# Kernel optimization log

Measured on AMD Instinct MI355X. Metric: run time of the kernel, lower is better.

## Reference

```python
import jax, jax.numpy as jnp
import numpy as np

B, T, C, H, M, R = 2, 2048, 768, 6, 3072, 320
D = C // H  # head_dim = 128


def setup_inputs() -> dict:
    key = jax.random.key(0)
    ks = jax.random.split(key, 11)
    s = 0.02
    return {
        "x": jax.random.normal(ks[0], (B, T, C), jnp.float32),
        "forward_memory": jax.random.normal(ks[1], (B, M, C), jnp.float32),
        "reverse_memory": jax.random.normal(ks[2], (B, R, C), jnp.float32),
        "ctrl": jax.random.uniform(ks[3], (5,), jnp.float32),
        "Wq": jax.random.normal(ks[4], (C, C), jnp.float32) * s,
        "Wk": jax.random.normal(ks[5], (C, C), jnp.float32) * s,
        "Wv": jax.random.normal(ks[6], (C, C), jnp.float32) * s,
        "Wo": jax.random.normal(ks[7], (C, C), jnp.float32) * s,
        "Wc": jax.random.normal(ks[8], (C, 5), jnp.float32) * 1e-4,  # ctrl_init_scale
        "Wg": jax.random.normal(ks[9], (H, C), jnp.float32) * s,
        "bg": jnp.full((H,), -1.0, jnp.float32),  # gate_bias_init
    }


def reference(x, forward_memory, reverse_memory, ctrl, Wq, Wk, Wv, Wo, Wc, Wg, bg):
    Bx, Tx, Cx = x.shape
    Hx = bg.shape[0]
    Dx = Cx // Hx
    # query with control-vector fusion (ctrl broadcast to every token)
    q = x @ Wq.T + ctrl @ Wc.T  # [B,T,C]
    # concat local tokens with forward+reverse memory, project K/V once
    kv_in = jnp.concatenate([x, forward_memory, reverse_memory], axis=1)  # [B,S,C]
    k = kv_in @ Wk.T
    v = kv_in @ Wv.T

    def heads(t):
        return t.reshape(Bx, -1, Hx, Dx).transpose(0, 2, 1, 3)  # [B,H,*,D]

    qh, kh, vh = heads(q), heads(k), heads(v)
    S = kh.shape[2]
    scores = jnp.einsum("bhtd,bhsd->bhts", qh, kh) * (Dx ** -0.5)
    # causal mask over local block only; memory columns always visible
    causal = jnp.triu(jnp.ones((Tx, Tx), bool), 1)
    mask = jnp.concatenate([causal, jnp.zeros((Tx, S - Tx), bool)], axis=1)
    scores = jnp.where(mask, jnp.float32(-1e30), scores)
    w = jax.nn.softmax(scores, axis=-1)  # [B,H,T,S]
    # split attention output into local and memory contributions
    local = jnp.einsum("bhts,bhsd->bhtd", w[..., :Tx], vh[:, :, :Tx])
    mem = jnp.einsum("bhts,bhsd->bhtd", w[..., Tx:], vh[:, :, Tx:])
    # per-head sigmoid gate on the memory path, computed from the fused query
    gate = jax.nn.sigmoid(q @ Wg.T + bg)  # [B,T,H]
    gate = gate.transpose(0, 2, 1)[..., None]  # [B,H,T,1]
    out = local + gate * mem
    out = out.transpose(0, 2, 1, 3).reshape(Bx, Tx, Cx)
    return out @ Wo.T
```

## Files before the change

kernel.cpp:

```cpp
#include <hip/hip_runtime.h>


typedef unsigned short u16;
typedef unsigned int   u32;
typedef __bf16 bf16x8 __attribute__((ext_vector_type(8)));
typedef float  f32x4  __attribute__((ext_vector_type(4)));

#define B_ 2
#define T_ 2048
#define C_ 768
#define H_ 6
#define D_ 128
#define M_ 3072
#define R_ 320
#define S_ 5440
#define BT_ 4096
#define BS_ 10880
#define NS_ 4
#define NMEM_ 53

#define GLDS(src, dst) __builtin_amdgcn_global_load_lds( \
    (const __attribute__((address_space(1))) void*)(src), \
    (__attribute__((address_space(3))) void*)(dst), 16, 0, 0)

__device__ __forceinline__ float b2f(u16 u) {
  union { u32 i; float f; } c; c.i = ((u32)u) << 16; return c.f;
}
__device__ __forceinline__ u16 f2b(float f) {
  union { float f; u32 i; } c; c.f = f;
  return (u16)((c.i + 0x7FFFu + ((c.i >> 16) & 1u)) >> 16);
}

__global__ __launch_bounds__(256) void k_cast4(const float* __restrict__ s0,
                                               const float* __restrict__ s1,
                                               const float* __restrict__ s2,
                                               const float* __restrict__ s3,
                                               u16* __restrict__ d0,
                                               u16* __restrict__ d1,
                                               u16* __restrict__ d2,
                                               u16* __restrict__ d3) {
  const float* src = (blockIdx.y == 0) ? s0 : (blockIdx.y == 1) ? s1
                   : (blockIdx.y == 2) ? s2 : s3;
  u16* dst = (blockIdx.y == 0) ? d0 : (blockIdx.y == 1) ? d1
           : (blockIdx.y == 2) ? d2 : d3;
  int i = (blockIdx.x * 256 + threadIdx.x) * 4;
  float4 v = *(const float4*)(src + i);
  u16 o[4] = { f2b(v.x), f2b(v.y), f2b(v.z), f2b(v.w) };
  *(ushort4*)(dst + i) = *(ushort4*)o;
}

__global__ __launch_bounds__(256) void k_concat(const float* __restrict__ x,
                                                const float* __restrict__ fm,
                                                const float* __restrict__ rm,
                                                u16* __restrict__ kv) {
  long long i = ((long long)blockIdx.x * 256 + threadIdx.x) * 8;
  if (i >= (long long)BS_ * C_) return;
  int row = (int)(i / C_);
  int col = (int)(i - (long long)row * C_);
  int b = row / S_, s = row - b * S_;
  const float* src;
  if (s < T_)           src = x  + (size_t)(b * T_ + s) * C_ + col;
  else if (s < T_ + M_) src = fm + (size_t)(b * M_ + (s - T_)) * C_ + col;
  else                  src = rm + (size_t)(b * R_ + (s - T_ - M_)) * C_ + col;
  float4 a0 = *(const float4*)src;
  float4 a1 = *(const float4*)(src + 4);
  u16 o[8] = { f2b(a0.x), f2b(a0.y), f2b(a0.z), f2b(a0.w),
               f2b(a1.x), f2b(a1.y), f2b(a1.z), f2b(a1.w) };
  *(uint4*)(kv + i) = *(uint4*)o;
}

template<bool F32OUT, bool QCBIAS>
__global__ __launch_bounds__(256) void k_gemm(const u16* __restrict__ A,
                                              const u16* __restrict__ W,
                                              const float* __restrict__ ctrl,
                                              const float* __restrict__ Wc,
                                              void* __restrict__ outv,
                                              int rows, int rowShift, int bstride) {
  __shared__ __align__(16) u16 As[3][128 * 32];
  __shared__ __align__(16) u16 Bs[3][128 * 32];
  const int t = threadIdx.x;
  const int lane = t & 63, wv = t >> 6;
  const int wr = (wv >> 1) * 64, wc = (wv & 1) * 64;
  const int fr = lane & 15, fq = lane >> 4;
  const int rowTile = blockIdx.x * 128;
  const int colTile = blockIdx.y * 128;

  f32x4 acc[4][4] = {};

  const int e0 = t * 8;
  const int e1 = (256 + t) * 8;
  const int r0 = e0 >> 5, c0 = e0 & 31;
  const int r1 = e1 >> 5, c1 = e1 & 31;

  int gr0 = rowTile + r0; if (gr0 >= rows) gr0 = rows - 1;
  int gr1 = rowTile + r1; if (gr1 >= rows) gr1 = rows - 1;
  const int msk = (1 << rowShift) - 1;
  const size_t pr0 = (size_t)(gr0 >> rowShift) * bstride + (gr0 & msk);
  const size_t pr1 = (size_t)(gr1 >> rowShift) * bstride + (gr1 & msk);
  const u16* gaB0 = A + pr0 * C_ + c0;
  const u16* gaB1 = A + pr1 * C_ + c1;
  const u16* gbB0 = W + (size_t)(colTile + r0) * C_ + c0;
  const u16* gbB1 = W + (size_t)(colTile + r1) * C_ + c1;
  const int aOff0 = (wv * 64) * 8, aOff1 = (256 + wv * 64) * 8;

#define STAGE_G(bi, kt) do { \
    GLDS(gaB0 + (kt), &As[bi][aOff0]); \
    GLDS(gaB1 + (kt), &As[bi][aOff1]); \
    GLDS(gbB0 + (kt), &Bs[bi][aOff0]); \
    GLDS(gbB1 + (kt), &Bs[bi][aOff1]); } while (0)

  STAGE_G(0, 0);
  STAGE_G(1, 32);
  int cur = 0;

  for (int kt = 0; kt < C_; kt += 32) {
    int nx2 = cur + 2; if (nx2 >= 3) nx2 -= 3;
    if (kt + 64 < C_) {
      STAGE_G(nx2, kt + 64);
      asm volatile("s_waitcnt vmcnt(8)" ::: "memory");
    } else if (kt + 32 < C_) {
      asm volatile("s_waitcnt vmcnt(4)" ::: "memory");
    } else {
      asm volatile("s_waitcnt vmcnt(0)" ::: "memory");
    }
    __builtin_amdgcn_s_barrier();

    bf16x8 af[4], bfr[4];
#pragma unroll
    for (int i = 0; i < 4; ++i) af[i]  = *(const bf16x8*)&As[cur][(wr + i * 16 + fr) * 32 + fq * 8];
#pragma unroll
    for (int i = 0; i < 4; ++i) bfr[i] = *(const bf16x8*)&Bs[cur][(wc + i * 16 + fr) * 32 + fq * 8];
#pragma unroll
    for (int mi = 0; mi < 4; ++mi)
#pragma unroll
      for (int ni = 0; ni < 4; ++ni)
        acc[mi][ni] = __builtin_amdgcn_mfma_f32_16x16x32_bf16(af[mi], bfr[ni], acc[mi][ni], 0, 0, 0);
    __builtin_amdgcn_s_barrier();
    cur = (cur == 2) ? 0 : cur + 1;
  }
#undef STAGE_G

#pragma unroll
  for (int mi = 0; mi < 4; ++mi) {
#pragma unroll
    for (int ni = 0; ni < 4; ++ni) {
      int cc = colTile + wc + ni * 16 + fr;
      float bb = 0.f;
      if (QCBIAS) {
#pragma unroll
        for (int j = 0; j < 5; ++j) bb += ctrl[j] * Wc[cc * 5 + j];
      }
#pragma unroll
      for (int j = 0; j < 4; ++j) {
        int rr = rowTile + wr + mi * 16 + fq * 4 + j;
        if (rr < rows) {
          float val = acc[mi][ni][j] + bb;
          if (F32OUT) ((float*)outv)[(size_t)rr * C_ + cc] = val;
          else        ((u16*)outv)[(size_t)rr * C_ + cc] = f2b(val);
        }
      }
    }
  }
}

__global__ __launch_bounds__(256, 2) void k_gemmKV(const u16* __restrict__ kvb,
                                                   const u16* __restrict__ Wk,
                                                   const u16* __restrict__ Wv,
                                                   u16* __restrict__ kb,
                                                   u16* __restrict__ vt) {
  __shared__ __align__(16) u16 As[2][128 * 32];
  __shared__ __align__(16) u16 Ks2[2][128 * 32];
  __shared__ __align__(16) u16 Vs2[2][128 * 32];
  const int t = threadIdx.x;
  const int lane = t & 63, wv = t >> 6;
  const int wr = (wv >> 1) * 64, wc = (wv & 1) * 64;
  const int fr = lane & 15, fq = lane >> 4;
  const int rowTile = blockIdx.x * 128;
  const int colTile = blockIdx.y * 128;

  f32x4 accK[4][4] = {};
  f32x4 accV[4][4] = {};

  const int e0 = t * 8;
  const int e1 = (256 + t) * 8;
  const int r0 = e0 >> 5, c0 = e0 & 31;
  const int r1 = e1 >> 5, c1 = e1 & 31;

  const u16* gaB0 = kvb + (size_t)(rowTile + r0) * C_ + c0;
  const u16* gaB1 = kvb + (size_t)(rowTile + r1) * C_ + c1;
  const u16* gkB0 = Wk + (size_t)(colTile + r0) * C_ + c0;
  const u16* gkB1 = Wk + (size_t)(colTile + r1) * C_ + c1;
  const u16* gvB0 = Wv + (size_t)(colTile + r0) * C_ + c0;
  const u16* gvB1 = Wv + (size_t)(colTile + r1) * C_ + c1;
  const int aOff0 = (wv * 64) * 8, aOff1 = (256 + wv * 64) * 8;

#define STAGE_KV(bi, kt) do { \
    GLDS(gaB0 + (kt), &As[bi][aOff0]); \
    GLDS(gaB1 + (kt), &As[bi][aOff1]); \
    GLDS(gkB0 + (kt), &Ks2[bi][aOff0]); \
    GLDS(gkB1 + (kt), &Ks2[bi][aOff1]); \
    GLDS(gvB0 + (kt), &Vs2[bi][aOff0]); \
    GLDS(gvB1 + (kt), &Vs2[bi][aOff1]); } while (0)

  STAGE_KV(0, 0);
  int cur = 0;

  for (int kt = 0; kt < C_; kt += 32) {
    if (kt + 32 < C_) {
      STAGE_KV(cur ^ 1, kt + 32);
      asm volatile("s_waitcnt vmcnt(6)" ::: "memory");
    } else {
      asm volatile("s_waitcnt vmcnt(0)" ::: "memory");
    }
    __builtin_amdgcn_s_barrier();

    bf16x8 af[4], wkf[4], wvf[4];
#pragma unroll
    for (int i = 0; i < 4; ++i) af[i]  = *(const bf16x8*)&As[cur][(wr + i * 16 + fr) * 32 + fq * 8];
#pragma unroll
    for (int i = 0; i < 4; ++i) wkf[i] = *(const bf16x8*)&Ks2[cur][(wc + i * 16 + fr) * 32 + fq * 8];
#pragma unroll
    for (int i = 0; i < 4; ++i) wvf[i] = *(const bf16x8*)&Vs2[cur][(wc + i * 16 + fr) * 32 + fq * 8];
#pragma unroll
    for (int mi = 0; mi < 4; ++mi)
#pragma unroll
      for (int ni = 0; ni < 4; ++ni) {
        accK[mi][ni] = __builtin_amdgcn_mfma_f32_16x16x32_bf16(af[mi], wkf[ni], accK[mi][ni], 0, 0, 0);
        accV[mi][ni] = __builtin_amdgcn_mfma_f32_16x16x32_bf16(wvf[mi], af[ni], accV[mi][ni], 0, 0, 0);
      }
    __builtin_amdgcn_s_barrier();
    cur ^= 1;
  }
#undef STAGE_KV

#pragma unroll
  for (int mi = 0; mi < 4; ++mi) {
#pragma unroll
    for (int ni = 0; ni < 4; ++ni) {
      int cc = colTile + wc + ni * 16 + fr;
#pragma unroll
      for (int j = 0; j < 4; ++j) {
        int rr = rowTile + wr + mi * 16 + fq * 4 + j;
        kb[(size_t)rr * C_ + cc] = f2b(accK[mi][ni][j]);
      }
    }
  }
#pragma unroll
  for (int mi = 0; mi < 4; ++mi) {
#pragma unroll
    for (int ni = 0; ni < 4; ++ni) {
      int sg = rowTile + wr + ni * 16 + fr;
      int b = sg / S_, s = sg - b * S_;
#pragma unroll
      for (int j = 0; j < 4; ++j) {
        int cc = colTile + wc + mi * 16 + fq * 4 + j;
        vt[((size_t)(b * C_ + cc)) * S_ + s] = f2b(accV[mi][ni][j]);
      }
    }
  }
}

__global__ __launch_bounds__(256) void k_gate(const u16* __restrict__ q,
                                              const float* __restrict__ Wg,
                                              const float* __restrict__ bg,
                                              float* __restrict__ gate) {
  int gid = blockIdx.x * 4 + (threadIdx.x >> 6);
  int lane = threadIdx.x & 63;
  int h = gid % H_;
  int bt = gid / H_;
  const u16* qrow = q + (size_t)bt * C_;
  const float* wrow = Wg + (size_t)h * C_;
  float a = 0.f;
#pragma unroll
  for (int i = 0; i < 12; ++i) {
    int e = i * 64 + lane;
    a += b2f(qrow[e]) * wrow[e];
  }
#pragma unroll
  for (int off = 1; off < 64; off <<= 1) a += __shfl_xor(a, off);
  if (lane == 0) {
    float xg = a + bg[h];
    int b = bt / T_, tt = bt - b * T_;
    gate[((size_t)b * H_ + h) * T_ + tt] = 1.f / (1.f + __expf(-xg));
  }
}

__global__ __launch_bounds__(512, 4) void k_attn8(const u16* __restrict__ q,
                                                  const u16* __restrict__ kk,
                                                  const u16* __restrict__ vt,
                                                  const float* __restrict__ gate,
                                                  u16* __restrict__ pacc0,
                                                  u16* __restrict__ pacc1,
                                                  u16* __restrict__ pacc2,
                                                  u16* __restrict__ pacc3,
                                                  float* __restrict__ pl) {
  __shared__ __align__(16) u16 Ks[2][64 * 128];
  __shared__ __align__(16) u16 Vs[128 * 64];
  __shared__ __align__(16) u16 Pb[8][16 * 64];

  const int bh = blockIdx.x;
  const int b = bh / H_, h = bh - b * H_;
  const int y = 15 - blockIdx.y;
  const int c = blockIdx.z;
  const int wv = threadIdx.x >> 6, lane = threadIdx.x & 63;
  const int fr = lane & 15, fq = lane >> 4;
  const int qbase = y * 128 + wv * 16;
  char* Pc = (char*)Pb[wv];

  const u16* Qh = q + (size_t)(b * T_ + qbase) * C_ + h * D_;
  const float* gh = gate + ((size_t)b * H_ + h) * T_ + qbase;

  const int kRow0 = wv * 8 + (lane >> 4), kRow1 = kRow0 + 4;
  const int kCol0 = (((lane & 15) * 16) ^ ((kRow0 & 7) << 4)) >> 1;
  const int kCol1 = (((lane & 15) * 16) ^ ((kRow1 & 7) << 4)) >> 1;
  const u16* kSrc0 = kk + (size_t)(b * S_ + kRow0) * C_ + h * D_ + kCol0;
  const u16* kSrc1 = kk + (size_t)(b * S_ + kRow1) * C_ + h * D_ + kCol1;
  const int vRow0 = wv * 16 + (lane >> 3), vRow1 = vRow0 + 8;
  const int vCol0 = (((lane & 7) * 16) ^ ((vRow0 & 7) << 4)) >> 1;
  const int vCol1 = (((lane & 7) * 16) ^ ((vRow1 & 7) << 4)) >> 1;
  const u16* vSrc0 = vt + ((size_t)b * C_ + h * D_ + vRow0) * S_ + vCol0;
  const u16* vSrc1 = vt + ((size_t)b * C_ + h * D_ + vRow1) * S_ + vCol1;

  bf16x8 qf[4];
#pragma unroll
  for (int kc = 0; kc < 4; ++kc)
    qf[kc] = *(const bf16x8*)&Qh[(size_t)fr * C_ + kc * 32 + fq * 8];

  f32x4 acc[8] = {};
  f32x4 accL = {}, accM = {};
  float g4[4], lg[4];
#pragma unroll
  for (int r = 0; r < 4; ++r) { g4[r] = gh[fq * 4 + r]; lg[r] = __log2f(g4[r]); }

  const __bf16 one_h = (__bf16)1.0f;
  bf16x8 ones = { one_h, one_h, one_h, one_h, one_h, one_h, one_h, one_h };

  const float scl = 0.08838834764831845f * 1.4426950408889634f;
  const int xk = (fr & 7) << 4;

  const int nloc = 2 * y + 2;
  const int ntot = nloc + NMEM_;
  auto s_of = [&](int i) { return (i < nloc) ? i * 64 : T_ + (i - nloc) * 64; };

  {
    int s0 = s_of(c);
    GLDS(kSrc0 + (size_t)s0 * C_, &Ks[0][(wv * 8) * 128]);
    GLDS(kSrc1 + (size_t)s0 * C_, &Ks[0][(wv * 8 + 4) * 128]);
  }
  int cur = 0;

  for (int i = c; i < ntot; i += NS_) {
    const int s0 = s_of(i);
    const bool haveNext = (i + NS_ < ntot);
    GLDS(vSrc0 + s0, &Vs[(wv * 16) * 64]);
    GLDS(vSrc1 + s0, &Vs[(wv * 16 + 8) * 64]);
    if (haveNext) {
      int sn = s_of(i + NS_);
      GLDS(kSrc0 + (size_t)sn * C_, &Ks[cur ^ 1][(wv * 8) * 128]);
      GLDS(kSrc1 + (size_t)sn * C_, &Ks[cur ^ 1][(wv * 8 + 4) * 128]);
      asm volatile("s_waitcnt vmcnt(4)" ::: "memory");
    } else {
      asm volatile("s_waitcnt vmcnt(2)" ::: "memory");
    }
    __builtin_amdgcn_s_barrier();

    const bool loc = (i < nloc);
    const bool maskedStep = loc && (s0 + 63 > qbase);
    const bool skip = loc && (s0 > qbase + 15);

    bf16x8 pa0, pa1;
    if (!skip) {
      f32x4 sc[4] = {{}, {}, {}, {}};
#pragma unroll
      for (int quad = 0; quad < 4; ++quad) {
        const u16* Krow = &Ks[cur][(quad * 16 + fr) * 128];
#pragma unroll
        for (int kc = 0; kc < 4; ++kc) {
          bf16x8 kf = *(const bf16x8*)&Krow[((kc * 64 + fq * 16) ^ xk) >> 1];
          sc[quad] = __builtin_amdgcn_mfma_f32_16x16x32_bf16(qf[kc], kf, sc[quad], 0, 0, 0);
        }
      }
      if (maskedStep) {
#pragma unroll
        for (int quad = 0; quad < 4; ++quad)
#pragma unroll
          for (int r = 0; r < 4; ++r)
            if (s0 + quad * 16 + fr > qbase + fq * 4 + r) sc[quad][r] = -1.0e30f;
      }
      float ca[4];
#pragma unroll
      for (int r = 0; r < 4; ++r) ca[r] = loc ? 0.f : lg[r];
#pragma unroll
      for (int quad = 0; quad < 4; ++quad)
#pragma unroll
        for (int r = 0; r < 4; ++r) {
          int row = fq * 4 + r;
          int cb = (quad * 32 + fr * 2) ^ ((row & 7) << 4);
          *(__bf16*)(Pc + row * 128 + cb) =
              (__bf16)exp2f(fmaf(sc[quad][r], scl, ca[r]));
        }
      __builtin_amdgcn_wave_barrier();
      pa0 = *(const bf16x8*)(Pc + fr * 128 + ((fq * 16) ^ ((fr & 7) << 4)));
      pa1 = *(const bf16x8*)(Pc + fr * 128 + ((64 + fq * 16) ^ ((fr & 7) << 4)));
    }
    if (haveNext) asm volatile("s_waitcnt vmcnt(2)" ::: "memory");
    else          asm volatile("s_waitcnt vmcnt(0)" ::: "memory");
    __builtin_amdgcn_s_barrier();
    if (!skip) {
#pragma unroll
      for (int nt = 0; nt < 8; ++nt) {
        const u16* Vrow = &Vs[(nt * 16 + fr) * 64];
        bf16x8 vf0 = *(const bf16x8*)&Vrow[((fq * 16) ^ xk) >> 1];
        bf16x8 vf1 = *(const bf16x8*)&Vrow[((64 + fq * 16) ^ xk) >> 1];
        acc[nt] = __builtin_amdgcn_mfma_f32_16x16x32_bf16(pa0, vf0, acc[nt], 0, 0, 0);
        acc[nt] = __builtin_amdgcn_mfma_f32_16x16x32_bf16(pa1, vf1, acc[nt], 0, 0, 0);
      }
      if (loc) {
        accL = __builtin_amdgcn_mfma_f32_16x16x32_bf16(pa0, ones, accL, 0, 0, 0);
        accL = __builtin_amdgcn_mfma_f32_16x16x32_bf16(pa1, ones, accL, 0, 0, 0);
      } else {
        accM = __builtin_amdgcn_mfma_f32_16x16x32_bf16(pa0, ones, accM, 0, 0, 0);
        accM = __builtin_amdgcn_mfma_f32_16x16x32_bf16(pa1, ones, accM, 0, 0, 0);
      }
    }
    __builtin_amdgcn_s_barrier();
    cur ^= 1;
  }

  u16* pb = (c == 0) ? pacc0 : (c == 1) ? pacc1 : (c == 2) ? pacc2 : pacc3;
  const size_t rowb = (size_t)bh * T_ + qbase;
#pragma unroll
  for (int nt = 0; nt < 8; ++nt)
#pragma unroll
    for (int r = 0; r < 4; ++r)
      ((__bf16*)pb)[(rowb + fq * 4 + r) * D_ + nt * 16 + fr] = (__bf16)acc[nt][r];
  if (fr == 0) {
#pragma unroll
    for (int r = 0; r < 4; ++r)
      pl[((size_t)c * (B_ * H_) + bh) * T_ + qbase + fq * 4 + r] =
          accL[r] + accM[r] / g4[r];
  }
}

__global__ __launch_bounds__(256) void k_combine(const u16* __restrict__ pacc0,
                                                 const u16* __restrict__ pacc1,
                                                 const u16* __restrict__ pacc2,
                                                 const u16* __restrict__ pacc3,
                                                 const float* __restrict__ pl,
                                                 u16* __restrict__ ao) {
  const int row = blockIdx.x * 4 + (threadIdx.x >> 6);
  const int lane = threadIdx.x & 63;
  const int bh = row >> 11, t = row & (T_ - 1);
  const int b = bh / H_, h = bh - b * H_;

  float L = pl[(size_t)bh * T_ + t]
          + pl[((size_t)(B_ * H_) + bh) * T_ + t]
          + pl[((size_t)(2 * B_ * H_) + bh) * T_ + t]
          + pl[((size_t)(3 * B_ * H_) + bh) * T_ + t];
  float inv = 1.f / L;
  const size_t rb = ((size_t)bh * T_ + t) * D_ + lane * 2;
  u32 v0 = *(const u32*)&pacc0[rb];
  u32 v1 = *(const u32*)&pacc1[rb];
  u32 v2 = *(const u32*)&pacc2[rb];
  u32 v3 = *(const u32*)&pacc3[rb];
  float o0 = b2f((u16)(v0 & 0xFFFF)) + b2f((u16)(v1 & 0xFFFF))
           + b2f((u16)(v2 & 0xFFFF)) + b2f((u16)(v3 & 0xFFFF));
  float o1 = b2f((u16)(v0 >> 16)) + b2f((u16)(v1 >> 16))
           + b2f((u16)(v2 >> 16)) + b2f((u16)(v3 >> 16));
  u16 o[2] = { f2b(o0 * inv), f2b(o1 * inv) };
  *(u32*)&ao[((size_t)(b * T_ + t)) * C_ + h * D_ + lane * 2] = *(u32*)o;
}

extern "C" void kernel_launch(void* const* d_in, const int* in_sizes, int n_in,
                              void* d_out, int out_size, void* d_ws, size_t ws_size,
                              hipStream_t stream) {
  const float* x   = (const float*)d_in[0];
  const float* fm  = (const float*)d_in[1];
  const float* rm  = (const float*)d_in[2];
  const float* ctl = (const float*)d_in[3];
  const float* Wq  = (const float*)d_in[4];
  const float* Wk  = (const float*)d_in[5];
  const float* Wv  = (const float*)d_in[6];
  const float* Wo  = (const float*)d_in[7];
  const float* Wc  = (const float*)d_in[8];
  const float* Wg  = (const float*)d_in[9];
  const float* bg  = (const float*)d_in[10];
  float* outp = (float*)d_out;

  char* ws = (char*)d_ws;
  float* gate = (float*)(ws + 4096);
  u16* qb    = (u16*)(ws + 102400);
  u16* kv    = (u16*)(ws + 6393856);
  u16* pacc0 = (u16*)(ws + 6393856);
  u16* pacc1 = (u16*)(ws + 12685312);
  u16* kb    = (u16*)(ws + 23105536);
  u16* vt    = (u16*)(ws + 39817216);
  u16* ao    = (u16*)(ws + 39817216);
  u16* pacc2 = (u16*)(ws + 56528896);
  u16* pacc3 = (u16*)(ws + 62820352);
  float* pl  = (float*)(ws + 69111808);
  u16* Wqb   = (u16*)(ws + 69505024);
  u16* Wkb   = (u16*)(ws + 70684672);
  u16* Wvb   = (u16*)(ws + 71864320);
  u16* Wob   = (u16*)(ws + 73043968);

  k_cast4<<<dim3(576, 4), dim3(256), 0, stream>>>(Wq, Wk, Wv, Wo,
                                                  Wqb, Wkb, Wvb, Wob);
  k_concat<<<dim3(4080), dim3(256), 0, stream>>>(x, fm, rm, kv);
  k_gemm<false, true><<<dim3(32, 6), dim3(256), 0, stream>>>(
      kv, Wqb, ctl, Wc, qb, BT_, 11, S_);
  k_gemmKV<<<dim3(85, 6), dim3(256), 0, stream>>>(kv, Wkb, Wvb, kb, vt);
  k_gate<<<dim3(6144), dim3(256), 0, stream>>>(qb, Wg, bg, gate);
  k_attn8<<<dim3(B_ * H_, 16, NS_), dim3(512), 0, stream>>>(
      qb, kb, vt, gate, pacc0, pacc1, pacc2, pacc3, pl);
  k_combine<<<dim3(6144), dim3(256), 0, stream>>>(pacc0, pacc1, pacc2, pacc3, pl, ao);
  k_gemm<true, false><<<dim3(32, 6), dim3(256), 0, stream>>>(
      ao, Wob, nullptr, nullptr, outp, BT_, 30, 0);
}
```

Before: 212.1 us.

## Process 32 query rows per wave in attention to reuse K/V fragments

The attention kernel now has each wave handle two 16-row query tiles (256 rows per block instead of 128), halving the grid's y dimension. Each K and V fragment read from LDS feeds two MFMAs, which roughly halves LDS traffic and global K/V staging per query row. In exchange, register pressure doubles for accumulators and Q fragments under launch_bounds(512,4), which risks spills or lower occupancy. It also halves the number of blocks and coarsens causal skipping, so more work lands on masked tiles.

```diff
diff --git a/kernel.cpp b/kernel.cpp
--- a/kernel.cpp
+++ b/kernel.cpp
@@ -22,6 +22,8 @@
 #define GLDS(src, dst) __builtin_amdgcn_global_load_lds( \
     (const __attribute__((address_space(1))) void*)(src), \
     (__attribute__((address_space(3))) void*)(dst), 16, 0, 0)
+
+#define MFMA16(a, b, c) __builtin_amdgcn_mfma_f32_16x16x32_bf16((a), (b), (c), 0, 0, 0)
 
 __device__ __forceinline__ float b2f(u16 u) {
   union { u32 i; float f; } c; c.i = ((u32)u) << 16; return c.f;
@@ -134,7 +136,7 @@
     for (int mi = 0; mi < 4; ++mi)
 #pragma unroll
       for (int ni = 0; ni < 4; ++ni)
-        acc[mi][ni] = __builtin_amdgcn_mfma_f32_16x16x32_bf16(af[mi], bfr[ni], acc[mi][ni], 0, 0, 0);
+        acc[mi][ni] = MFMA16(af[mi], bfr[ni], acc[mi][ni]);
     __builtin_amdgcn_s_barrier();
     cur = (cur == 2) ? 0 : cur + 1;
   }
@@ -225,8 +227,8 @@
     for (int mi = 0; mi < 4; ++mi)
 #pragma unroll
       for (int ni = 0; ni < 4; ++ni) {
-        accK[mi][ni] = __builtin_amdgcn_mfma_f32_16x16x32_bf16(af[mi], wkf[ni], accK[mi][ni], 0, 0, 0);
-        accV[mi][ni] = __builtin_amdgcn_mfma_f32_16x16x32_bf16(wvf[mi], af[ni], accV[mi][ni], 0, 0, 0);
+        accK[mi][ni] = MFMA16(af[mi], wkf[ni], accK[mi][ni]);
+        accV[mi][ni] = MFMA16(wvf[mi], af[ni], accV[mi][ni]);
       }
     __builtin_amdgcn_s_barrier();
     cur ^= 1;
@@ -285,7 +287,7 @@
   }
 }
 
-__global__ __launch_bounds__(512, 4) void k_attn8(const u16* __restrict__ q,
+__global__ __launch_bounds__(512, 4) void k_attn9(const u16* __restrict__ q,
                                                   const u16* __restrict__ kk,
                                                   const u16* __restrict__ vt,
                                                   const float* __restrict__ gate,
@@ -296,15 +298,15 @@
                                                   float* __restrict__ pl) {
   __shared__ __align__(16) u16 Ks[2][64 * 128];
   __shared__ __align__(16) u16 Vs[128 * 64];
-  __shared__ __align__(16) u16 Pb[8][16 * 64];
+  __shared__ __align__(16) u16 Pb[8][32 * 64];
 
   const int bh = blockIdx.x;
   const int b = bh / H_, h = bh - b * H_;
-  const int y = 15 - blockIdx.y;
+  const int y = 7 - blockIdx.y;
   const int c = blockIdx.z;
   const int wv = threadIdx.x >> 6, lane = threadIdx.x & 63;
   const int fr = lane & 15, fq = lane >> 4;
-  const int qbase = y * 128 + wv * 16;
+  const int qbase = y * 256 + wv * 32;
   char* Pc = (char*)Pb[wv];
 
   const u16* Qh = q + (size_t)(b * T_ + qbase) * C_ + h * D_;
@@ -321,24 +323,30 @@
   const u16* vSrc0 = vt + ((size_t)b * C_ + h * D_ + vRow0) * S_ + vCol0;
   const u16* vSrc1 = vt + ((size_t)b * C_ + h * D_ + vRow1) * S_ + vCol1;
 
-  bf16x8 qf[4];
-#pragma unroll
-  for (int kc = 0; kc < 4; ++kc)
-    qf[kc] = *(const bf16x8*)&Qh[(size_t)fr * C_ + kc * 32 + fq * 8];
-
-  f32x4 acc[8] = {};
-  f32x4 accL = {}, accM = {};
-  float g4[4], lg[4];
-#pragma unroll
-  for (int r = 0; r < 4; ++r) { g4[r] = gh[fq * 4 + r]; lg[r] = __log2f(g4[r]); }
+  bf16x8 qf0[4], qf1[4];
+#pragma unroll
+  for (int kc = 0; kc < 4; ++kc) {
+    qf0[kc] = *(const bf16x8*)&Qh[(size_t)fr * C_ + kc * 32 + fq * 8];
+    qf1[kc] = *(const bf16x8*)&Qh[(size_t)(16 + fr) * C_ + kc * 32 + fq * 8];
+  }
+
+  f32x4 acc0[8] = {}, acc1[8] = {};
+  f32x4 accL0 = {}, accM0 = {}, accL1 = {}, accM1 = {};
+  float g0[4], lg0[4], g1[4], lg1[4];
+#pragma unroll
+  for (int r = 0; r < 4; ++r) {
+    g0[r] = gh[fq * 4 + r];      lg0[r] = __log2f(g0[r]);
+    g1[r] = gh[16 + fq * 4 + r]; lg1[r] = __log2f(g1[r]);
+  }
 
   const __bf16 one_h = (__bf16)1.0f;
   bf16x8 ones = { one_h, one_h, one_h, one_h, one_h, one_h, one_h, one_h };
 
   const float scl = 0.08838834764831845f * 1.4426950408889634f;
   const int xk = (fr & 7) << 4;
-
-  const int nloc = 2 * y + 2;
+  const int xp = (fr & 7) << 4;
+
+  const int nloc = 4 * y + 4;
   const int ntot = nloc + NMEM_;
   auto s_of = [&](int i) { return (i < nloc) ? i * 64 : T_ + (i - nloc) * 64; };
 
@@ -366,42 +374,50 @@
 
     const bool loc = (i < nloc);
     const bool maskedStep = loc && (s0 + 63 > qbase);
-    const bool skip = loc && (s0 > qbase + 15);
-
-    bf16x8 pa0, pa1;
+    const bool skip = loc && (s0 > qbase + 31);
+
+    bf16x8 pa00, pa01, pa10, pa11;
     if (!skip) {
-      f32x4 sc[4] = {{}, {}, {}, {}};
+      f32x4 sc0[4] = {{}, {}, {}, {}};
+      f32x4 sc1[4] = {{}, {}, {}, {}};
 #pragma unroll
       for (int quad = 0; quad < 4; ++quad) {
         const u16* Krow = &Ks[cur][(quad * 16 + fr) * 128];
 #pragma unroll
         for (int kc = 0; kc < 4; ++kc) {
           bf16x8 kf = *(const bf16x8*)&Krow[((kc * 64 + fq * 16) ^ xk) >> 1];
-          sc[quad] = __builtin_amdgcn_mfma_f32_16x16x32_bf16(qf[kc], kf, sc[quad], 0, 0, 0);
+          sc0[quad] = MFMA16(qf0[kc], kf, sc0[quad]);
+          sc1[quad] = MFMA16(qf1[kc], kf, sc1[quad]);
         }
       }
       if (maskedStep) {
 #pragma unroll
         for (int quad = 0; quad < 4; ++quad)
 #pragma unroll
-          for (int r = 0; r < 4; ++r)
-            if (s0 + quad * 16 + fr > qbase + fq * 4 + r) sc[quad][r] = -1.0e30f;
-      }
-      float ca[4];
-#pragma unroll
-      for (int r = 0; r < 4; ++r) ca[r] = loc ? 0.f : lg[r];
+          for (int r = 0; r < 4; ++r) {
+            int col = s0 + quad * 16 + fr;
+            if (col > qbase + fq * 4 + r)      sc0[quad][r] = -1.0e30f;
+            if (col > qbase + 16 + fq * 4 + r) sc1[quad][r] = -1.0e30f;
+          }
+      }
 #pragma unroll
       for (int quad = 0; quad < 4; ++quad)
 #pragma unroll
         for (int r = 0; r < 4; ++r) {
           int row = fq * 4 + r;
           int cb = (quad * 32 + fr * 2) ^ ((row & 7) << 4);
+          float ca0 = loc ? 0.f : lg0[r];
+          float ca1 = loc ? 0.f : lg1[r];
           *(__bf16*)(Pc + row * 128 + cb) =
-              (__bf16)exp2f(fmaf(sc[quad][r], scl, ca[r]));
+              (__bf16)exp2f(fmaf(sc0[quad][r], scl, ca0));
+          *(__bf16*)(Pc + (16 + row) * 128 + cb) =
+              (__bf16)exp2f(fmaf(sc1[quad][r], scl, ca1));
         }
       __builtin_amdgcn_wave_barrier();
-      pa0 = *(const bf16x8*)(Pc + fr * 128 + ((fq * 16) ^ ((fr & 7) << 4)));
-      pa1 = *(const bf16x8*)(Pc + fr * 128 + ((64 + fq * 16) ^ ((fr & 7) << 4)));
+      pa00 = *(const bf16x8*)(Pc + fr * 128 + ((fq * 16) ^ xp));
+      pa01 = *(const bf16x8*)(Pc + fr * 128 + ((64 + fq * 16) ^ xp));
+      pa10 = *(const bf16x8*)(Pc + (16 + fr) * 128 + ((fq * 16) ^ xp));
+      pa11 = *(const bf16x8*)(Pc + (16 + fr) * 128 + ((64 + fq * 16) ^ xp));
     }
     if (haveNext) asm volatile("s_waitcnt vmcnt(2)" ::: "memory");
     else          asm volatile("s_waitcnt vmcnt(0)" ::: "memory");
@@ -412,15 +428,21 @@
         const u16* Vrow = &Vs[(nt * 16 + fr) * 64];
         bf16x8 vf0 = *(const bf16x8*)&Vrow[((fq * 16) ^ xk) >> 1];
         bf16x8 vf1 = *(const bf16x8*)&Vrow[((64 + fq * 16) ^ xk) >> 1];
-        acc[nt] = __builtin_amdgcn_mfma_f32_16x16x32_bf16(pa0, vf0, acc[nt], 0, 0, 0);
-        acc[nt] = __builtin_amdgcn_mfma_f32_16x16x32_bf16(pa1, vf1, acc[nt], 0, 0, 0);
+        acc0[nt] = MFMA16(pa00, vf0, acc0[nt]);
+        acc0[nt] = MFMA16(pa01, vf1, acc0[nt]);
+        acc1[nt] = MFMA16(pa10, vf0, acc1[nt]);
+        acc1[nt] = MFMA16(pa11, vf1, acc1[nt]);
       }
       if (loc) {
-        accL = __builtin_amdgcn_mfma_f32_16x16x32_bf16(pa0, ones, accL, 0, 0, 0);
-        accL = __builtin_amdgcn_mfma_f32_16x16x32_bf16(pa1, ones, accL, 0, 0, 0);
+        accL0 = MFMA16(pa00, ones, accL0);
+        accL0 = MFMA16(pa01, ones, accL0);
+        accL1 = MFMA16(pa10, ones, accL1);
+        accL1 = MFMA16(pa11, ones, accL1);
       } else {
-        accM = __builtin_amdgcn_mfma_f32_16x16x32_bf16(pa0, ones, accM, 0, 0, 0);
-        accM = __builtin_amdgcn_mfma_f32_16x16x32_bf16(pa1, ones, accM, 0, 0, 0);
+        accM0 = MFMA16(pa00, ones, accM0);
+        accM0 = MFMA16(pa01, ones, accM0);
+        accM1 = MFMA16(pa10, ones, accM1);
+        accM1 = MFMA16(pa11, ones, accM1);
       }
     }
     __builtin_amdgcn_s_barrier();
@@ -432,13 +454,17 @@
 #pragma unroll
   for (int nt = 0; nt < 8; ++nt)
 #pragma unroll
-    for (int r = 0; r < 4; ++r)
-      ((__bf16*)pb)[(rowb + fq * 4 + r) * D_ + nt * 16 + fr] = (__bf16)acc[nt][r];
+    for (int r = 0; r < 4; ++r) {
+      ((__bf16*)pb)[(rowb + fq * 4 + r) * D_ + nt * 16 + fr] = (__bf16)acc0[nt][r];
+      ((__bf16*)pb)[(rowb + 16 + fq * 4 + r) * D_ + nt * 16 + fr] = (__bf16)acc1[nt][r];
+    }
   if (fr == 0) {
-#pragma unroll
-    for (int r = 0; r < 4; ++r)
-      pl[((size_t)c * (B_ * H_) + bh) * T_ + qbase + fq * 4 + r] =
-          accL[r] + accM[r] / g4[r];
+    const size_t plb = ((size_t)c * (B_ * H_) + bh) * T_ + qbase;
+#pragma unroll
+    for (int r = 0; r < 4; ++r) {
+      pl[plb + fq * 4 + r]      = accL0[r] + accM0[r] / g0[r];
+      pl[plb + 16 + fq * 4 + r] = accL1[r] + accM1[r] / g1[r];
+    }
   }
 }
 
@@ -511,7 +537,7 @@
       kv, Wqb, ctl, Wc, qb, BT_, 11, S_);
   k_gemmKV<<<dim3(85, 6), dim3(256), 0, stream>>>(kv, Wkb, Wvb, kb, vt);
   k_gate<<<dim3(6144), dim3(256), 0, stream>>>(qb, Wg, bg, gate);
-  k_attn8<<<dim3(B_ * H_, 16, NS_), dim3(512), 0, stream>>>(
+  k_attn9<<<dim3(B_ * H_, 8, NS_), dim3(512), 0, stream>>>(
       qb, kb, vt, gate, pacc0, pacc1, pacc2, pacc3, pl);
   k_combine<<<dim3(6144), dim3(256), 0, stream>>>(pacc0, pacc1, pacc2, pacc3, pl, ao);
   k_gemm<true, false><<<dim3(32, 6), dim3(256), 0, stream>>>(
```

New measurement: 457.0 us. 115% more time.
